# Kernel optimization log

Measured on AMD Instinct MI355X. Metric: run time of the kernel, lower is better.

The kernel has to match this reference:

```python
import jax, jax.numpy as jnp
import numpy as np

BATCH, SEQ, INPUT_SIZE, RESERVOIR = 32, 2048, 256, 512


def setup_inputs() -> dict:
    key = jax.random.key(0)
    k_x, k_w, k_d = jax.random.split(key, 3)
    x = jax.random.normal(k_x, (BATCH, SEQ, INPUT_SIZE), dtype=jnp.float32)
    # input_projection weight: uniform(-1, 1), shape [R, input_size]
    W_in = jax.random.uniform(k_w, (RESERVOIR, INPUT_SIZE), dtype=jnp.float32, minval=-1.0, maxval=1.0)
    # diagonal of state_projection: uniform(-0.5, 0.5)
    d = jax.random.uniform(k_d, (RESERVOIR,), dtype=jnp.float32, minval=-0.5, maxval=0.5)
    return {"x": x, "W_in": W_in, "d": d}


def reference(x, W_in, d):
    B, T, _ = x.shape
    R = d.shape[0]
    # input projection: [B, T, R]
    u = jnp.einsum('bti,ri->btr', x, W_in)

    # recurrence: state_t = tanh(d * state_{t-1} + u_t)  (leak gate is dead code: 0*old + 1*new)
    # torch loop fills indices 1..T-1 of all_states (T+1 slots), then returns [:, 1:],
    # so the final returned timestep is all zeros.
    def step(state, u_t):
        new_state = jnp.tanh(d * state + u_t)
        return new_state, new_state

    init = jnp.zeros((B, R), dtype=x.dtype)
    u_tm = jnp.swapaxes(u[:, 1:, :], 0, 1)  # time-major [T-1, B, R]
    _, states = jax.lax.scan(step, init, u_tm)
    states = jnp.swapaxes(states, 0, 1)  # [B, T-1, R]
    tail = jnp.zeros((B, 1, R), dtype=x.dtype)
    return jnp.concatenate([states, tail], axis=1)  # [B, T, R]
```

## Files before the change

### kernel.cpp

```cpp
#include <hip/hip_runtime.h>

#define BATCH 32
#define SEQT  2048
#define INSZ  256
#define RSV   512
#define MTOT  (BATCH * SEQT)
#define BM 128
#define BN 128
#define BK 32
#define NK  (INSZ / BK)
#define LSA 40
#define LOPLANE 131072

#define K2LOG2E 2.8853900817779268f

using f16x8 = __attribute__((ext_vector_type(8))) _Float16;
using f16x4 = __attribute__((ext_vector_type(4))) _Float16;
using f32x4 = __attribute__((ext_vector_type(4))) float;

typedef __attribute__((address_space(1))) unsigned int as1_u32;
typedef __attribute__((address_space(3))) unsigned int as3_u32;
#define GLDS16(gp, lp) __builtin_amdgcn_global_load_lds((as1_u32*)(gp), (as3_u32*)(lp), 16, 0, 0)

static __device__ __forceinline__ float esn_step(float s, float u, float dK) {
    float z  = __builtin_fmaf(dK, s, u * K2LOG2E);
    float e  = __builtin_amdgcn_exp2f(z);
    float rc = __builtin_amdgcn_rcpf(1.0f + e);
    return __builtin_fmaf(-2.0f, rc, 1.0f);
}


__global__ __launch_bounds__(256) void esn_convw(const float* __restrict__ W,
                                                 _Float16* __restrict__ W16T) {
    const int i = blockIdx.x * 256 + threadIdx.x;
    const int bn = i >> 12, ks = (i >> 9) & 7, c = i & 511;
    const int q = c >> 7, row = c & 127;
    const float* src = W + (size_t)(bn * 128 + row) * INSZ + ks * 32 + q * 8;
    float4 v0 = *(const float4*)src;
    float4 v1 = *(const float4*)(src + 4);
    float w8[8] = {v0.x, v0.y, v0.z, v0.w, v1.x, v1.y, v1.z, v1.w};
    f16x8 h, l;
    #pragma unroll
    for (int j = 0; j < 8; ++j) {
        _Float16 hh = (_Float16)w8[j];
        h[j] = hh;
        l[j] = (_Float16)(w8[j] - (float)hh);
    }
    *(f16x8*)(W16T + (size_t)i * 8) = h;
    *(f16x8*)(W16T + LOPLANE + (size_t)i * 8) = l;
}

__global__ __launch_bounds__(256) void esn_gemm_f(const float* __restrict__ X,
                                                  const _Float16* __restrict__ W16T,
                                                  _Float16* __restrict__ U16) {
    __shared__ _Float16 Bh[2][4096];
    __shared__ _Float16 Bl[2][4096];

    const int tid  = threadIdx.x;
    const int lane = tid & 63;
    const int wid  = tid >> 6;
    const int wr   = wid >> 1, wc = wid & 1;
    const int lgc = (blockIdx.x & 7) * 256 + (blockIdx.x >> 3);
    const int bm = lgc >> 2, bn = lgc & 3;

    const float* xbase = X + (size_t)(bm * BM + wr * 64 + (lane & 15)) * INSZ + (lane >> 4) * 8;

    f32x4 acc[4][4] = {};
    f16x8 af[4];

    #pragma unroll
    for (int j = 0; j < 2; ++j) {
        const int cb = (wid * 2 + j) * 64;
        const _Float16* gh = W16T + ((size_t)(bn * 8 + 0) * 512 + cb + lane) * 8;
        GLDS16(gh, &Bh[0][cb * 8]);
        GLDS16(gh + LOPLANE, &Bl[0][cb * 8]);
    }
    #pragma unroll
    for (int m = 0; m < 4; ++m) {
        const float* xp = xbase + m * 16 * INSZ;
        float4 x0 = *(const float4*)xp;
        float4 x1 = *(const float4*)(xp + 4);
        float x8[8] = {x0.x, x0.y, x0.z, x0.w, x1.x, x1.y, x1.z, x1.w};
        #pragma unroll
        for (int j = 0; j < 8; ++j) af[m][j] = (_Float16)x8[j];
    }
    __syncthreads();

    #pragma unroll
    for (int ks = 0; ks < NK; ++ks) {
        const int cur = ks & 1, nxt = cur ^ 1;
        float4 xr[4][2];
        if (ks + 1 < NK) {
            #pragma unroll
            for (int j = 0; j < 2; ++j) {
                const int cb = (wid * 2 + j) * 64;
                const _Float16* gh = W16T + ((size_t)(bn * 8 + ks + 1) * 512 + cb + lane) * 8;
                GLDS16(gh, &Bh[nxt][cb * 8]);
                GLDS16(gh + LOPLANE, &Bl[nxt][cb * 8]);
            }
            #pragma unroll
            for (int m = 0; m < 4; ++m) {
                const float* xp = xbase + m * 16 * INSZ + (ks + 1) * BK;
                xr[m][0] = *(const float4*)xp;
                xr[m][1] = *(const float4*)(xp + 4);
            }
        }
        f16x8 bfh[4], bfl[4];
        #pragma unroll
        for (int n = 0; n < 4; ++n) {
            const int rr = (lane >> 4) * 1024 + (wc * 64 + n * 16 + (lane & 15)) * 8;
            bfh[n] = *(const f16x8*)&Bh[cur][rr];
            bfl[n] = *(const f16x8*)&Bl[cur][rr];
        }
        #pragma unroll
        for (int m = 0; m < 4; ++m)
            #pragma unroll
            for (int n = 0; n < 4; ++n) {
                acc[m][n] = __builtin_amdgcn_mfma_f32_16x16x32_f16(bfh[n], af[m], acc[m][n], 0, 0, 0);
                acc[m][n] = __builtin_amdgcn_mfma_f32_16x16x32_f16(bfl[n], af[m], acc[m][n], 0, 0, 0);
            }
        if (ks + 1 < NK) {
            #pragma unroll
            for (int m = 0; m < 4; ++m) {
                float x8[8] = {xr[m][0].x, xr[m][0].y, xr[m][0].z, xr[m][0].w,
                               xr[m][1].x, xr[m][1].y, xr[m][1].z, xr[m][1].w};
                #pragma unroll
                for (int j = 0; j < 8; ++j) af[m][j] = (_Float16)x8[j];
            }
        }
        __syncthreads();
    }

    #pragma unroll
    for (int m = 0; m < 4; ++m) {
        const int gm = bm * BM + wr * 64 + m * 16 + (lane & 15);
        #pragma unroll
        for (int n = 0; n < 4; ++n) {
            const int gr = bn * BN + wc * 64 + n * 16 + (lane >> 4) * 4;
            f32x4 v = acc[m][n];
            f16x4 o;
            #pragma unroll
            for (int j = 0; j < 4; ++j) o[j] = (_Float16)v[j];
            *(f16x4*)(U16 + (size_t)gm * RSV + gr) = o;
        }
    }
}

__global__ __launch_bounds__(256) void esn_recur_f(const _Float16* __restrict__ U16,
                                                   const float* __restrict__ D,
                                                   float* __restrict__ OUT) {
    const int tid  = threadIdx.x;
    const int b    = blockIdx.x >> 5;
    const int seg  = (blockIdx.x >> 1) & 15;
    const int half = blockIdx.x & 1;
    const int r    = half * 256 + tid;

    const _Float16* ub = U16 + (size_t)b * SEQT * RSV + r;
    float* ob = OUT + (size_t)b * SEQT * RSV + r;
    const float dK = D[r] * K2LOG2E;
    const int t0 = seg * 128;

    float s = 0.0f;
    if (seg) {
        #pragma unroll 8
        for (int k = 0; k < 32; ++k)
            s = esn_step(s, (float)ub[(size_t)(t0 - 31 + k) * RSV], dK);
    }

    _Float16 bufA[8], bufB[8];
    #pragma unroll
    for (int j = 0; j < 8; ++j) bufA[j] = ub[(size_t)(t0 + 1 + j) * RSV];
    #pragma unroll
    for (int j = 0; j < 8; ++j) bufB[j] = ub[(size_t)(t0 + 9 + j) * RSV];

#define PROC8F(buf, tt) do {                                  \
    _Pragma("unroll")                                         \
    for (int j = 0; j < 8; ++j) {                             \
        s = esn_step(s, (float)buf[j], dK);                   \
        ob[(size_t)((tt) + j) * RSV] = s;                     \
        int idx = (tt) + j + 17;                              \
        idx = idx < SEQT ? idx : SEQT - 1;                    \
        buf[j] = ub[(size_t)idx * RSV];                       \
    }                                                         \
} while (0)

    int t = t0;
    for (int it = 0; it < 8; ++it) {
        PROC8F(bufA, t);
        PROC8F(bufB, t + 8);
        t += 16;
    }
#undef PROC8F
    if (seg == 15) ob[(size_t)(SEQT - 1) * RSV] = 0.0f;
}


__global__ __launch_bounds__(256) void esn_gemm_fb(const float* __restrict__ X,
                                                   const float* __restrict__ W,
                                                   float* __restrict__ U) {
    __shared__ _Float16 Ash[BM * LSA];
    __shared__ _Float16 Bsh[BN * 72];

    const int tid  = threadIdx.x;
    const int lane = tid & 63;
    const int wid  = tid >> 6;
    const int wr   = wid >> 1, wc = wid & 1;
    const int bm   = blockIdx.x >> 2, bn = blockIdx.x & 3;
    const int srow = tid >> 3;
    const int scol = (tid & 7) * 4;

    f32x4 acc[4][4] = {};

    for (int ks = 0; ks < NK; ++ks) {
        __syncthreads();
        #pragma unroll
        for (int p = 0; p < 4; ++p) {
            const int row = srow + p * 32;
            float4 av = *(const float4*)(X + (size_t)(bm * BM + row) * INSZ + ks * BK + scol);
            float4 bv = *(const float4*)(W + (size_t)(bn * BN + row) * INSZ + ks * BK + scol);
            float a4[4] = {av.x, av.y, av.z, av.w};
            float b4[4] = {bv.x, bv.y, bv.z, bv.w};
            f16x4 ah, bh, bl;
            #pragma unroll
            for (int j = 0; j < 4; ++j) {
                ah[j] = (_Float16)a4[j];
                _Float16 h = (_Float16)b4[j];
                bh[j] = h;
                bl[j] = (_Float16)(b4[j] - (float)h);
            }
            *(f16x4*)&Ash[row * LSA + scol] = ah;
            *(f16x4*)&Bsh[row * 72 + scol] = bh;
            *(f16x4*)&Bsh[row * 72 + 32 + scol] = bl;
        }
        __syncthreads();

        f16x8 af[4], bfh[4], bfl[4];
        #pragma unroll
        for (int m = 0; m < 4; ++m)
            af[m] = *(const f16x8*)&Ash[(wr * 64 + m * 16 + (lane & 15)) * LSA + (lane >> 4) * 8];
        #pragma unroll
        for (int n = 0; n < 4; ++n) {
            const _Float16* p = &Bsh[(wc * 64 + n * 16 + (lane & 15)) * 72 + (lane >> 4) * 8];
            bfh[n] = *(const f16x8*)p;
            bfl[n] = *(const f16x8*)(p + 32);
        }
        #pragma unroll
        for (int m = 0; m < 4; ++m)
            #pragma unroll
            for (int n = 0; n < 4; ++n) {
                acc[m][n] = __builtin_amdgcn_mfma_f32_16x16x32_f16(af[m], bfh[n], acc[m][n], 0, 0, 0);
                acc[m][n] = __builtin_amdgcn_mfma_f32_16x16x32_f16(af[m], bfl[n], acc[m][n], 0, 0, 0);
            }
    }

    #pragma unroll
    for (int m = 0; m < 4; ++m) {
        const int row = bm * BM + wr * 64 + m * 16 + (lane >> 4) * 4;
        #pragma unroll
        for (int n = 0; n < 4; ++n) {
            const int col = bn * BN + wc * 64 + n * 16 + (lane & 15);
            f32x4 v = acc[m][n];
            #pragma unroll
            for (int j = 0; j < 4; ++j)
                U[(size_t)(row + j) * RSV + col] = v[j];
        }
    }
}

__global__ __launch_bounds__(64) void esn_recur_fb(float* __restrict__ OUT,
                                                   const float* __restrict__ D) {
    const int gid = blockIdx.x * 64 + threadIdx.x;
    const int b = gid >> 9;
    const int r = gid & (RSV - 1);
    float* base = OUT + (size_t)b * SEQT * RSV + r;
    const float dK = D[r] * K2LOG2E;
    float s = 0.0f;

    float bA[8], bB[8], bC[8], bD[8];
    #pragma unroll
    for (int j = 0; j < 8; ++j) bA[j] = base[(size_t)(1 + j) * RSV];
    #pragma unroll
    for (int j = 0; j < 8; ++j) bB[j] = base[(size_t)(9 + j) * RSV];
    #pragma unroll
    for (int j = 0; j < 8; ++j) bC[j] = base[(size_t)(17 + j) * RSV];
    #pragma unroll
    for (int j = 0; j < 8; ++j) bD[j] = base[(size_t)(25 + j) * RSV];

#define PROC8B(buf, tt) do {                                  \
    _Pragma("unroll")                                         \
    for (int j = 0; j < 8; ++j) {                             \
        s = esn_step(s, buf[j], dK);                          \
        base[(size_t)((tt) + j) * RSV] = s;                   \
        int idx = (tt) + 33 + j;                              \
        idx = idx < SEQT ? idx : SEQT - 1;                    \
        buf[j] = base[(size_t)idx * RSV];                     \
    }                                                         \
} while (0)

    int t = 0;
    for (int it = 0; it < 63; ++it) {
        PROC8B(bA, t);
        PROC8B(bB, t + 8);
        PROC8B(bC, t + 16);
        PROC8B(bD, t + 24);
        t += 32;
    }
#undef PROC8B
    #pragma unroll
    for (int j = 0; j < 8; ++j) { s = esn_step(s, bA[j], dK); base[(size_t)(2016 + j) * RSV] = s; }
    #pragma unroll
    for (int j = 0; j < 8; ++j) { s = esn_step(s, bB[j], dK); base[(size_t)(2024 + j) * RSV] = s; }
    #pragma unroll
    for (int j = 0; j < 8; ++j) { s = esn_step(s, bC[j], dK); base[(size_t)(2032 + j) * RSV] = s; }
    #pragma unroll
    for (int j = 0; j < 7; ++j) { s = esn_step(s, bD[j], dK); base[(size_t)(2040 + j) * RSV] = s; }

    base[(size_t)(SEQT - 1) * RSV] = 0.0f;
}

extern "C" void kernel_launch(void* const* d_in, const int* in_sizes, int n_in,
                              void* d_out, int out_size, void* d_ws, size_t ws_size,
                              hipStream_t stream) {
    const float* X = (const float*)d_in[0];
    const float* W = (const float*)d_in[1];
    const float* D = (const float*)d_in[2];
    float* OUT = (float*)d_out;

    const size_t W16T_BYTES = (size_t)2 * RSV * INSZ * sizeof(_Float16);
    const size_t U16_BYTES  = (size_t)MTOT * RSV * sizeof(_Float16);
    if (ws_size >= W16T_BYTES + U16_BYTES) {
        _Float16* W16T = (_Float16*)d_ws;
        _Float16* U16  = (_Float16*)((char*)d_ws + W16T_BYTES);
        esn_convw<<<dim3(64), dim3(256), 0, stream>>>(W, W16T);
        esn_gemm_f<<<dim3((MTOT / BM) * (RSV / BN)), dim3(256), 0, stream>>>(X, W16T, U16);
        esn_recur_f<<<dim3(BATCH * 16 * 2), dim3(256), 0, stream>>>(U16, D, OUT);
    } else {
        esn_gemm_fb<<<dim3((MTOT / BM) * (RSV / BN)), dim3(256), 0, stream>>>(X, W, OUT);
        esn_recur_fb<<<dim3(BATCH * RSV / 64), dim3(64), 0, stream>>>(OUT, D);
    }
}
```

Baseline: 281.6 us.

## Keep full-K weight slice resident in LDS and stream X rows per wave

The GEMM now tiles 512 rows by 64 columns. It loads the whole K=256 hi/lo fp16 weight slice (64 KB) into LDS once per block, which removes the per-K-step double-buffered B loads and barriers. Each wave then processes its 128 rows in chunks of 32, keeping X register prefetch two K-steps ahead and converting X to fp16 on the fly. The weight packing kernel is re-laid out to match. In exchange, each block uses far more LDS and so lowers occupancy, each wave keeps fewer accumulators, and X is read from global with less reuse per tile.

```diff
diff --git a/kernel.cpp b/kernel.cpp
--- a/kernel.cpp
+++ b/kernel.cpp
@@ -5,10 +5,8 @@
 #define INSZ  256
 #define RSV   512
 #define MTOT  (BATCH * SEQT)
-#define BM 128
-#define BN 128
-#define BK 32
-#define NK  (INSZ / BK)
+#define BMR 512
+#define BNR 64
 #define LSA 40
 #define LOPLANE 131072
 
@@ -33,9 +31,9 @@
 __global__ __launch_bounds__(256) void esn_convw(const float* __restrict__ W,
                                                  _Float16* __restrict__ W16T) {
     const int i = blockIdx.x * 256 + threadIdx.x;
-    const int bn = i >> 12, ks = (i >> 9) & 7, c = i & 511;
-    const int q = c >> 7, row = c & 127;
-    const float* src = W + (size_t)(bn * 128 + row) * INSZ + ks * 32 + q * 8;
+    const int bn = i >> 11, c = i & 2047;
+    const int ks = c >> 8, q = (c >> 6) & 3, r = c & 63;
+    const float* src = W + (size_t)(bn * BNR + r) * INSZ + ks * 32 + q * 8;
     float4 v0 = *(const float4*)src;
     float4 v1 = *(const float4*)(src + 4);
     float w8[8] = {v0.x, v0.y, v0.z, v0.w, v1.x, v1.y, v1.z, v1.w};
@@ -53,95 +51,76 @@
 __global__ __launch_bounds__(256) void esn_gemm_f(const float* __restrict__ X,
                                                   const _Float16* __restrict__ W16T,
                                                   _Float16* __restrict__ U16) {
-    __shared__ _Float16 Bh[2][4096];
-    __shared__ _Float16 Bl[2][4096];
+    __shared__ _Float16 Wsh[2 * 16384];
 
     const int tid  = threadIdx.x;
     const int lane = tid & 63;
     const int wid  = tid >> 6;
-    const int wr   = wid >> 1, wc = wid & 1;
-    const int lgc = (blockIdx.x & 7) * 256 + (blockIdx.x >> 3);
-    const int bm = lgc >> 2, bn = lgc & 3;
-
-    const float* xbase = X + (size_t)(bm * BM + wr * 64 + (lane & 15)) * INSZ + (lane >> 4) * 8;
-
-    f32x4 acc[4][4] = {};
-    f16x8 af[4];
-
-    #pragma unroll
-    for (int j = 0; j < 2; ++j) {
-        const int cb = (wid * 2 + j) * 64;
-        const _Float16* gh = W16T + ((size_t)(bn * 8 + 0) * 512 + cb + lane) * 8;
-        GLDS16(gh, &Bh[0][cb * 8]);
-        GLDS16(gh + LOPLANE, &Bl[0][cb * 8]);
-    }
-    #pragma unroll
-    for (int m = 0; m < 4; ++m) {
-        const float* xp = xbase + m * 16 * INSZ;
-        float4 x0 = *(const float4*)xp;
-        float4 x1 = *(const float4*)(xp + 4);
-        float x8[8] = {x0.x, x0.y, x0.z, x0.w, x1.x, x1.y, x1.z, x1.w};
-        #pragma unroll
-        for (int j = 0; j < 8; ++j) af[m][j] = (_Float16)x8[j];
+    const int lg = (blockIdx.x & 7) * 128 + (blockIdx.x >> 3);
+    const int mg = lg >> 3, bn = lg & 7;
+
+    const _Float16* wsrc = W16T + (size_t)bn * 16384;
+    #pragma unroll
+    for (int i = 0; i < 8; ++i) {
+        const int cb = i * 256 + wid * 64;
+        GLDS16(wsrc + (size_t)(cb + lane) * 8, &Wsh[cb * 8]);
+        GLDS16(wsrc + LOPLANE + (size_t)(cb + lane) * 8, &Wsh[16384 + cb * 8]);
     }
     __syncthreads();
 
-    #pragma unroll
-    for (int ks = 0; ks < NK; ++ks) {
-        const int cur = ks & 1, nxt = cur ^ 1;
-        float4 xr[4][2];
-        if (ks + 1 < NK) {
-            #pragma unroll
-            for (int j = 0; j < 2; ++j) {
-                const int cb = (wid * 2 + j) * 64;
-                const _Float16* gh = W16T + ((size_t)(bn * 8 + ks + 1) * 512 + cb + lane) * 8;
-                GLDS16(gh, &Bh[nxt][cb * 8]);
-                GLDS16(gh + LOPLANE, &Bl[nxt][cb * 8]);
-            }
-            #pragma unroll
-            for (int m = 0; m < 4; ++m) {
-                const float* xp = xbase + m * 16 * INSZ + (ks + 1) * BK;
-                xr[m][0] = *(const float4*)xp;
-                xr[m][1] = *(const float4*)(xp + 4);
-            }
-        }
-        f16x8 bfh[4], bfl[4];
-        #pragma unroll
-        for (int n = 0; n < 4; ++n) {
-            const int rr = (lane >> 4) * 1024 + (wc * 64 + n * 16 + (lane & 15)) * 8;
-            bfh[n] = *(const f16x8*)&Bh[cur][rr];
-            bfl[n] = *(const f16x8*)&Bl[cur][rr];
-        }
-        #pragma unroll
-        for (int m = 0; m < 4; ++m)
-            #pragma unroll
-            for (int n = 0; n < 4; ++n) {
-                acc[m][n] = __builtin_amdgcn_mfma_f32_16x16x32_f16(bfh[n], af[m], acc[m][n], 0, 0, 0);
-                acc[m][n] = __builtin_amdgcn_mfma_f32_16x16x32_f16(bfl[n], af[m], acc[m][n], 0, 0, 0);
-            }
-        if (ks + 1 < NK) {
-            #pragma unroll
-            for (int m = 0; m < 4; ++m) {
-                float x8[8] = {xr[m][0].x, xr[m][0].y, xr[m][0].z, xr[m][0].w,
-                               xr[m][1].x, xr[m][1].y, xr[m][1].z, xr[m][1].w};
+    const int q = lane >> 4;
+    const float* xbase = X + (size_t)(mg * BMR + wid * 128 + (lane & 15)) * INSZ + q * 8;
+
+    for (int ch = 0; ch < 4; ++ch) {
+        f32x4 acc[2][4] = {};
+        float4 xrA[2][2], xrB[2][2];
+        #pragma unroll
+        for (int mf = 0; mf < 2; ++mf) {
+            const float* xp = xbase + (size_t)(ch * 32 + mf * 16) * INSZ;
+            xrA[mf][0] = *(const float4*)xp;       xrA[mf][1] = *(const float4*)(xp + 4);
+            xrB[mf][0] = *(const float4*)(xp + 32); xrB[mf][1] = *(const float4*)(xp + 36);
+        }
+        #pragma unroll
+        for (int ks = 0; ks < 8; ++ks) {
+            f16x8 af[2];
+            #pragma unroll
+            for (int mf = 0; mf < 2; ++mf) {
+                float4 x0 = (ks & 1) ? xrB[mf][0] : xrA[mf][0];
+                float4 x1 = (ks & 1) ? xrB[mf][1] : xrA[mf][1];
+                float x8[8] = {x0.x, x0.y, x0.z, x0.w, x1.x, x1.y, x1.z, x1.w};
                 #pragma unroll
-                for (int j = 0; j < 8; ++j) af[m][j] = (_Float16)x8[j];
-            }
-        }
-        __syncthreads();
-    }
-
-    #pragma unroll
-    for (int m = 0; m < 4; ++m) {
-        const int gm = bm * BM + wr * 64 + m * 16 + (lane & 15);
-        #pragma unroll
-        for (int n = 0; n < 4; ++n) {
-            const int gr = bn * BN + wc * 64 + n * 16 + (lane >> 4) * 4;
-            f32x4 v = acc[m][n];
-            f16x4 o;
-            #pragma unroll
-            for (int j = 0; j < 4; ++j) o[j] = (_Float16)v[j];
-            *(f16x4*)(U16 + (size_t)gm * RSV + gr) = o;
+                for (int j = 0; j < 8; ++j) af[mf][j] = (_Float16)x8[j];
+            }
+            if (ks + 2 < 8) {
+                #pragma unroll
+                for (int mf = 0; mf < 2; ++mf) {
+                    const float* xp = xbase + (size_t)(ch * 32 + mf * 16) * INSZ + (ks + 2) * 32;
+                    if (ks & 1) { xrB[mf][0] = *(const float4*)xp; xrB[mf][1] = *(const float4*)(xp + 4); }
+                    else        { xrA[mf][0] = *(const float4*)xp; xrA[mf][1] = *(const float4*)(xp + 4); }
+                }
+            }
+            #pragma unroll
+            for (int nf = 0; nf < 4; ++nf) {
+                const int coff = (((ks * 4 + q) * 64) + nf * 16 + (lane & 15)) * 8;
+                f16x8 wh = *(const f16x8*)&Wsh[coff];
+                f16x8 wl = *(const f16x8*)&Wsh[16384 + coff];
+                acc[0][nf] = __builtin_amdgcn_mfma_f32_16x16x32_f16(wh, af[0], acc[0][nf], 0, 0, 0);
+                acc[1][nf] = __builtin_amdgcn_mfma_f32_16x16x32_f16(wh, af[1], acc[1][nf], 0, 0, 0);
+                acc[0][nf] = __builtin_amdgcn_mfma_f32_16x16x32_f16(wl, af[0], acc[0][nf], 0, 0, 0);
+                acc[1][nf] = __builtin_amdgcn_mfma_f32_16x16x32_f16(wl, af[1], acc[1][nf], 0, 0, 0);
+            }
+        }
+        #pragma unroll
+        for (int mf = 0; mf < 2; ++mf) {
+            const int gm = mg * BMR + wid * 128 + ch * 32 + mf * 16 + (lane & 15);
+            #pragma unroll
+            for (int nf = 0; nf < 4; ++nf) {
+                const int gr = bn * BNR + nf * 16 + q * 4;
+                f16x4 o;
+                #pragma unroll
+                for (int j = 0; j < 4; ++j) o[j] = (_Float16)acc[mf][nf][j];
+                *(f16x4*)(U16 + (size_t)gm * RSV + gr) = o;
+            }
         }
     }
 }
@@ -198,8 +177,8 @@
 __global__ __launch_bounds__(256) void esn_gemm_fb(const float* __restrict__ X,
                                                    const float* __restrict__ W,
                                                    float* __restrict__ U) {
-    __shared__ _Float16 Ash[BM * LSA];
-    __shared__ _Float16 Bsh[BN * 72];
+    __shared__ _Float16 Ash[128 * LSA];
+    __shared__ _Float16 Bsh[128 * 72];
 
     const int tid  = threadIdx.x;
     const int lane = tid & 63;
@@ -211,13 +190,13 @@
 
     f32x4 acc[4][4] = {};
 
-    for (int ks = 0; ks < NK; ++ks) {
+    for (int ks = 0; ks < 8; ++ks) {
         __syncthreads();
         #pragma unroll
         for (int p = 0; p < 4; ++p) {
             const int row = srow + p * 32;
-            float4 av = *(const float4*)(X + (size_t)(bm * BM + row) * INSZ + ks * BK + scol);
-            float4 bv = *(const float4*)(W + (size_t)(bn * BN + row) * INSZ + ks * BK + scol);
+            float4 av = *(const float4*)(X + (size_t)(bm * 128 + row) * INSZ + ks * 32 + scol);
+            float4 bv = *(const float4*)(W + (size_t)(bn * 128 + row) * INSZ + ks * 32 + scol);
             float a4[4] = {av.x, av.y, av.z, av.w};
             float b4[4] = {bv.x, bv.y, bv.z, bv.w};
             f16x4 ah, bh, bl;
@@ -255,10 +234,10 @@
 
     #pragma unroll
     for (int m = 0; m < 4; ++m) {
-        const int row = bm * BM + wr * 64 + m * 16 + (lane >> 4) * 4;
+        const int row = bm * 128 + wr * 64 + m * 16 + (lane >> 4) * 4;
         #pragma unroll
         for (int n = 0; n < 4; ++n) {
-            const int col = bn * BN + wc * 64 + n * 16 + (lane & 15);
+            const int col = bn * 128 + wc * 64 + n * 16 + (lane & 15);
             f32x4 v = acc[m][n];
             #pragma unroll
             for (int j = 0; j < 4; ++j)
@@ -332,10 +311,10 @@
         _Float16* W16T = (_Float16*)d_ws;
         _Float16* U16  = (_Float16*)((char*)d_ws + W16T_BYTES);
         esn_convw<<<dim3(64), dim3(256), 0, stream>>>(W, W16T);
-        esn_gemm_f<<<dim3((MTOT / BM) * (RSV / BN)), dim3(256), 0, stream>>>(X, W16T, U16);
+        esn_gemm_f<<<dim3((MTOT / BMR) * (RSV / BNR)), dim3(256), 0, stream>>>(X, W16T, U16);
         esn_recur_f<<<dim3(BATCH * 16 * 2), dim3(256), 0, stream>>>(U16, D, OUT);
     } else {
-        esn_gemm_fb<<<dim3((MTOT / BM) * (RSV / BN)), dim3(256), 0, stream>>>(X, W, OUT);
+        esn_gemm_fb<<<dim3((MTOT / 128) * (RSV / 128)), dim3(256), 0, stream>>>(X, W, OUT);
         esn_recur_fb<<<dim3(BATCH * RSV / 64), dim3(64), 0, stream>>>(OUT, D);
     }
 }
```

After: 392.1 us. 39.3% more time.

## Stage X tiles through shared memory in GEMM and halve recurrence segments

Applied to the files above, without the earlier changes.

The GEMM kernel now loads X tiles cooperatively with coalesced row-wise float4 loads, converts them to fp16 and stages them in a double-buffered LDS array, instead of each wave loading its own strided fragments straight into registers. This cuts redundant global loads of X across the two column waves and improves coalescing, at the cost of extra LDS traffic and space. The recurrence kernel now uses 8 segments of 256 steps instead of 16 of 128. That halves the number of blocks and the redundant 32-step warm-up work, but lengthens each block's serial chain.

```diff
diff --git a/kernel.cpp b/kernel.cpp
--- a/kernel.cpp
+++ b/kernel.cpp
@@ -10,6 +10,7 @@
 #define BK 32
 #define NK  (INSZ / BK)
 #define LSA 40
+#define ASTR 1040
 #define LOPLANE 131072
 
 #define K2LOG2E 2.8853900817779268f
@@ -53,6 +54,7 @@
 __global__ __launch_bounds__(256) void esn_gemm_f(const float* __restrict__ X,
                                                   const _Float16* __restrict__ W16T,
                                                   _Float16* __restrict__ U16) {
+    __shared__ _Float16 Ash[2][4 * ASTR];
     __shared__ _Float16 Bh[2][4096];
     __shared__ _Float16 Bl[2][4096];
 
@@ -63,10 +65,12 @@
     const int lgc = (blockIdx.x & 7) * 256 + (blockIdx.x >> 3);
     const int bm = lgc >> 2, bn = lgc & 3;
 
-    const float* xbase = X + (size_t)(bm * BM + wr * 64 + (lane & 15)) * INSZ + (lane >> 4) * 8;
+    const int srow = tid >> 3;
+    const int scol = (tid & 7) * 4;
+    const int qa   = scol >> 3;
+    const int ha   = (scol >> 2) & 1;
 
     f32x4 acc[4][4] = {};
-    f16x8 af[4];
 
     #pragma unroll
     for (int j = 0; j < 2; ++j) {
@@ -76,20 +80,21 @@
         GLDS16(gh + LOPLANE, &Bl[0][cb * 8]);
     }
     #pragma unroll
-    for (int m = 0; m < 4; ++m) {
-        const float* xp = xbase + m * 16 * INSZ;
-        float4 x0 = *(const float4*)xp;
-        float4 x1 = *(const float4*)(xp + 4);
-        float x8[8] = {x0.x, x0.y, x0.z, x0.w, x1.x, x1.y, x1.z, x1.w};
-        #pragma unroll
-        for (int j = 0; j < 8; ++j) af[m][j] = (_Float16)x8[j];
+    for (int p = 0; p < 4; ++p) {
+        const int row = srow + p * 32;
+        float4 av = *(const float4*)(X + (size_t)(bm * BM + row) * INSZ + scol);
+        float a4[4] = {av.x, av.y, av.z, av.w};
+        f16x4 ah;
+        #pragma unroll
+        for (int j = 0; j < 4; ++j) ah[j] = (_Float16)a4[j];
+        *(f16x4*)&Ash[0][qa * ASTR + row * 8 + ha * 4] = ah;
     }
     __syncthreads();
 
     #pragma unroll
     for (int ks = 0; ks < NK; ++ks) {
         const int cur = ks & 1, nxt = cur ^ 1;
-        float4 xr[4][2];
+        float4 xr[4];
         if (ks + 1 < NK) {
             #pragma unroll
             for (int j = 0; j < 2; ++j) {
@@ -99,16 +104,20 @@
                 GLDS16(gh + LOPLANE, &Bl[nxt][cb * 8]);
             }
             #pragma unroll
-            for (int m = 0; m < 4; ++m) {
-                const float* xp = xbase + m * 16 * INSZ + (ks + 1) * BK;
-                xr[m][0] = *(const float4*)xp;
-                xr[m][1] = *(const float4*)(xp + 4);
-            }
-        }
-        f16x8 bfh[4], bfl[4];
+            for (int p = 0; p < 4; ++p) {
+                const int row = srow + p * 32;
+                xr[p] = *(const float4*)(X + (size_t)(bm * BM + row) * INSZ + (ks + 1) * BK + scol);
+            }
+        }
+
+        f16x8 af[4], bfh[4], bfl[4];
+        const int qf = lane >> 4;
+        #pragma unroll
+        for (int m = 0; m < 4; ++m)
+            af[m] = *(const f16x8*)&Ash[cur][qf * ASTR + (wr * 64 + m * 16 + (lane & 15)) * 8];
         #pragma unroll
         for (int n = 0; n < 4; ++n) {
-            const int rr = (lane >> 4) * 1024 + (wc * 64 + n * 16 + (lane & 15)) * 8;
+            const int rr = qf * 1024 + (wc * 64 + n * 16 + (lane & 15)) * 8;
             bfh[n] = *(const f16x8*)&Bh[cur][rr];
             bfl[n] = *(const f16x8*)&Bl[cur][rr];
         }
@@ -119,13 +128,16 @@
                 acc[m][n] = __builtin_amdgcn_mfma_f32_16x16x32_f16(bfh[n], af[m], acc[m][n], 0, 0, 0);
                 acc[m][n] = __builtin_amdgcn_mfma_f32_16x16x32_f16(bfl[n], af[m], acc[m][n], 0, 0, 0);
             }
+
         if (ks + 1 < NK) {
             #pragma unroll
-            for (int m = 0; m < 4; ++m) {
-                float x8[8] = {xr[m][0].x, xr[m][0].y, xr[m][0].z, xr[m][0].w,
-                               xr[m][1].x, xr[m][1].y, xr[m][1].z, xr[m][1].w};
+            for (int p = 0; p < 4; ++p) {
+                const int row = srow + p * 32;
+                float a4[4] = {xr[p].x, xr[p].y, xr[p].z, xr[p].w};
+                f16x4 ah;
                 #pragma unroll
-                for (int j = 0; j < 8; ++j) af[m][j] = (_Float16)x8[j];
+                for (int j = 0; j < 4; ++j) ah[j] = (_Float16)a4[j];
+                *(f16x4*)&Ash[nxt][qa * ASTR + row * 8 + ha * 4] = ah;
             }
         }
         __syncthreads();
@@ -137,10 +149,9 @@
         #pragma unroll
         for (int n = 0; n < 4; ++n) {
             const int gr = bn * BN + wc * 64 + n * 16 + (lane >> 4) * 4;
-            f32x4 v = acc[m][n];
             f16x4 o;
             #pragma unroll
-            for (int j = 0; j < 4; ++j) o[j] = (_Float16)v[j];
+            for (int j = 0; j < 4; ++j) o[j] = (_Float16)acc[m][n][j];
             *(f16x4*)(U16 + (size_t)gm * RSV + gr) = o;
         }
     }
@@ -150,15 +161,15 @@
                                                    const float* __restrict__ D,
                                                    float* __restrict__ OUT) {
     const int tid  = threadIdx.x;
-    const int b    = blockIdx.x >> 5;
-    const int seg  = (blockIdx.x >> 1) & 15;
+    const int b    = blockIdx.x >> 4;
+    const int seg  = (blockIdx.x >> 1) & 7;
     const int half = blockIdx.x & 1;
     const int r    = half * 256 + tid;
 
     const _Float16* ub = U16 + (size_t)b * SEQT * RSV + r;
     float* ob = OUT + (size_t)b * SEQT * RSV + r;
     const float dK = D[r] * K2LOG2E;
-    const int t0 = seg * 128;
+    const int t0 = seg * 256;
 
     float s = 0.0f;
     if (seg) {
@@ -185,21 +196,21 @@
 } while (0)
 
     int t = t0;
-    for (int it = 0; it < 8; ++it) {
+    for (int it = 0; it < 16; ++it) {
         PROC8F(bufA, t);
         PROC8F(bufB, t + 8);
         t += 16;
     }
 #undef PROC8F
-    if (seg == 15) ob[(size_t)(SEQT - 1) * RSV] = 0.0f;
+    if (seg == 7) ob[(size_t)(SEQT - 1) * RSV] = 0.0f;
 }
 
 
 __global__ __launch_bounds__(256) void esn_gemm_fb(const float* __restrict__ X,
                                                    const float* __restrict__ W,
                                                    float* __restrict__ U) {
-    __shared__ _Float16 Ash[BM * LSA];
-    __shared__ _Float16 Bsh[BN * 72];
+    __shared__ _Float16 Ash[128 * LSA];
+    __shared__ _Float16 Bsh[128 * 72];
 
     const int tid  = threadIdx.x;
     const int lane = tid & 63;
@@ -216,8 +227,8 @@
         #pragma unroll
         for (int p = 0; p < 4; ++p) {
             const int row = srow + p * 32;
-            float4 av = *(const float4*)(X + (size_t)(bm * BM + row) * INSZ + ks * BK + scol);
-            float4 bv = *(const float4*)(W + (size_t)(bn * BN + row) * INSZ + ks * BK + scol);
+            float4 av = *(const float4*)(X + (size_t)(bm * 128 + row) * INSZ + ks * 32 + scol);
+            float4 bv = *(const float4*)(W + (size_t)(bn * 128 + row) * INSZ + ks * 32 + scol);
             float a4[4] = {av.x, av.y, av.z, av.w};
             float b4[4] = {bv.x, bv.y, bv.z, bv.w};
             f16x4 ah, bh, bl;
@@ -255,10 +266,10 @@
 
     #pragma unroll
     for (int m = 0; m < 4; ++m) {
-        const int row = bm * BM + wr * 64 + m * 16 + (lane >> 4) * 4;
+        const int row = bm * 128 + wr * 64 + m * 16 + (lane >> 4) * 4;
         #pragma unroll
         for (int n = 0; n < 4; ++n) {
-            const int col = bn * BN + wc * 64 + n * 16 + (lane & 15);
+            const int col = bn * 128 + wc * 64 + n * 16 + (lane & 15);
             f32x4 v = acc[m][n];
             #pragma unroll
             for (int j = 0; j < 4; ++j)
@@ -333,9 +344,9 @@
         _Float16* U16  = (_Float16*)((char*)d_ws + W16T_BYTES);
         esn_convw<<<dim3(64), dim3(256), 0, stream>>>(W, W16T);
         esn_gemm_f<<<dim3((MTOT / BM) * (RSV / BN)), dim3(256), 0, stream>>>(X, W16T, U16);
-        esn_recur_f<<<dim3(BATCH * 16 * 2), dim3(256), 0, stream>>>(U16, D, OUT);
+        esn_recur_f<<<dim3(BATCH * 8 * 2), dim3(256), 0, stream>>>(U16, D, OUT);
     } else {
-        esn_gemm_fb<<<dim3((MTOT / BM) * (RSV / BN)), dim3(256), 0, stream>>>(X, W, OUT);
+        esn_gemm_fb<<<dim3((MTOT / 128) * (RSV / 128)), dim3(256), 0, stream>>>(X, W, OUT);
         esn_recur_fb<<<dim3(BATCH * RSV / 64), dim3(64), 0, stream>>>(OUT, D);
     }
 }
```

Result: faster. 271.6 us (-3.6%).
